# Performance work log

Hardware: AMD Instinct MI355X
Metric: run time of the kernel (lower is better)

## Reference

```python
import jax, jax.numpy as jnp
import numpy as np

HS = 1024
IMS = 4096
NHEAD = 16
EPS = 1e-5


def _layer_norm(x, g, b):
    mu = jnp.mean(x, axis=-1, keepdims=True)
    var = jnp.mean(jnp.square(x - mu), axis=-1, keepdims=True)
    return (x - mu) * jax.lax.rsqrt(var + EPS) * g + b


def setup_inputs() -> dict:
    key = jax.random.key(0)
    ks = jax.random.split(key, 10)
    B, S = 16, 512
    x = jax.random.normal(ks[0], (B, S, HS), dtype=jnp.float32)
    input_mask = jnp.zeros((B, S), dtype=jnp.float32)  # additive mask, 0 = attend
    sc = 0.02
    return {
        "x": x,
        "input_mask": input_mask,
        "qkv_w": jax.random.normal(ks[1], (3 * HS, HS), jnp.float32) * sc,
        "qkv_b": jnp.zeros((3 * HS,), jnp.float32),
        "attn_ow": jax.random.normal(ks[2], (HS, HS), jnp.float32) * sc,
        "attn_ob": jnp.zeros((HS,), jnp.float32),
        "ln1_g": jnp.ones((HS,), jnp.float32),
        "ln1_b": jnp.zeros((HS,), jnp.float32),
        "inter_w": jax.random.normal(ks[3], (IMS, HS), jnp.float32) * sc,
        "inter_b": jnp.zeros((IMS,), jnp.float32),
        "out_w": jax.random.normal(ks[4], (HS, IMS), jnp.float32) * sc,
        "out_b": jnp.zeros((HS,), jnp.float32),
        "ln2_g": jnp.ones((HS,), jnp.float32),
        "ln2_b": jnp.zeros((HS,), jnp.float32),
    }


def reference(x, input_mask, qkv_w, qkv_b, attn_ow, attn_ob, ln1_g, ln1_b,
              inter_w, inter_b, out_w, out_b, ln2_g, ln2_b):
    B, S, H = x.shape
    d = H // NHEAD
    # ---- self-attention block (pre_layer_norm=True, eval mode => no dropout) ----
    resid = x
    y = _layer_norm(x, ln1_g, ln1_b)
    qkv = jnp.einsum('bsh,eh->bse', y, qkv_w) + qkv_b  # [B,S,3H]
    q, k, v = jnp.split(qkv, 3, axis=-1)
    q = q.reshape(B, S, NHEAD, d)
    k = k.reshape(B, S, NHEAD, d)
    v = v.reshape(B, S, NHEAD, d)
    scores = jnp.einsum('bqnd,bknd->bnqk', q, k) / jnp.sqrt(jnp.float32(d))
    scores = scores + input_mask[:, None, None, :]  # additive padding mask
    probs = jax.nn.softmax(scores, axis=-1)
    ctx = jnp.einsum('bnqk,bknd->bqnd', probs, v).reshape(B, S, H)
    attn_out = jnp.einsum('bsh,oh->bso', ctx, attn_ow) + attn_ob
    x = resid + attn_out
    # ---- FFN block ----
    resid = x
    y = _layer_norm(x, ln2_g, ln2_b)
    h = jax.nn.relu(jnp.einsum('bsh,ih->bsi', y, inter_w) + inter_b)
    ffn_out = jnp.einsum('bsi,oi->bso', h, out_w) + out_b
    return resid + ffn_out
```

## Files before the change

### kernel.cpp

```cpp
#include <hip/hip_runtime.h>


using f32x4  = __attribute__((ext_vector_type(4))) float;
using f32x16 = __attribute__((ext_vector_type(16))) float;
using s16x8  = __attribute__((ext_vector_type(8))) short;
using i32x4  = __attribute__((ext_vector_type(4))) int;

__device__ __forceinline__ unsigned short f2bf(float f) {
    unsigned x = __builtin_bit_cast(unsigned, f);
    return (unsigned short)((x + 0x7fffu + ((x >> 16) & 1u)) >> 16);
}

#define GLL16(gptr, lptr)                                                     \
    __builtin_amdgcn_global_load_lds(                                         \
        (const __attribute__((address_space(1))) void*)(gptr),                \
        (__attribute__((address_space(3))) void*)(lptr), 16, 0, 0)

#define VMC(N) asm volatile("s_waitcnt vmcnt(" #N ")" ::: "memory")

__global__ __launch_bounds__(256) void wconv_kernel(
    const float* __restrict__ w0, const float* __restrict__ w1,
    const float* __restrict__ w2, const float* __restrict__ w3,
    unsigned short* __restrict__ o0, unsigned short* __restrict__ o1,
    unsigned short* __restrict__ o2, unsigned short* __restrict__ o3) {
    long idx = (long)blockIdx.x * 256 + threadIdx.x;
    const float* src;
    unsigned short* dst;
    long rel;
    if (idx < 786432L)        { src = w0; dst = o0; rel = idx; }
    else if (idx < 1048576L)  { src = w1; dst = o1; rel = idx - 786432L; }
    else if (idx < 2097152L)  { src = w2; dst = o2; rel = idx - 1048576L; }
    else                      { src = w3; dst = o3; rel = idx - 2097152L; }
    float4 v = *(const float4*)(src + rel * 4);
    ushort4 o;
    o.x = f2bf(v.x); o.y = f2bf(v.y); o.z = f2bf(v.z); o.w = f2bf(v.w);
    *(ushort4*)(dst + rel * 4) = o;
}

__global__ __launch_bounds__(256) void ln_kernel(
    const float* __restrict__ x, const float* __restrict__ gw,
    const float* __restrict__ bw, unsigned short* __restrict__ y) {
    __shared__ float rbuf[8];
    const int row = blockIdx.x;
    const int t = threadIdx.x;
    const float* xr = x + (size_t)row * 1024;
    float4 v = *(const float4*)(xr + t * 4);
    float s  = v.x + v.y + v.z + v.w;
    float ss = v.x * v.x + v.y * v.y + v.z * v.z + v.w * v.w;
#pragma unroll
    for (int sh = 1; sh < 64; sh <<= 1) {
        s  += __shfl_xor(s, sh, 64);
        ss += __shfl_xor(ss, sh, 64);
    }
    int w = t >> 6;
    if ((t & 63) == 0) { rbuf[w * 2] = s; rbuf[w * 2 + 1] = ss; }
    __syncthreads();
    s  = rbuf[0] + rbuf[2] + rbuf[4] + rbuf[6];
    ss = rbuf[1] + rbuf[3] + rbuf[5] + rbuf[7];
    float mu  = s * (1.f / 1024.f);
    float var = ss * (1.f / 1024.f) - mu * mu;
    float rs  = rsqrtf(var + 1e-5f);
    float4 gv = *(const float4*)(gw + t * 4);
    float4 bv = *(const float4*)(bw + t * 4);
    ushort4 o;
    o.x = f2bf((v.x - mu) * rs * gv.x + bv.x);
    o.y = f2bf((v.y - mu) * rs * gv.y + bv.y);
    o.z = f2bf((v.z - mu) * rs * gv.z + bv.z);
    o.w = f2bf((v.w - mu) * rs * gv.w + bv.w);
    *(ushort4*)(y + (size_t)row * 1024 + t * 4) = o;
}

template <bool RELU, bool RESID, bool OUT_BF16>
__global__ __launch_bounds__(256, 2) void gemm_bt(
    const unsigned short* __restrict__ A, const unsigned short* __restrict__ Bw,
    const float* __restrict__ bias, const float* __restrict__ resid,
    void* __restrict__ Cout, int M, int N, int K) {
    __shared__ char smem[2 * 128 * 64 * 2];
    char* As = smem;
    char* Bs = smem + 128 * 64 * 2;

    const int tid = threadIdx.x;
    const int lane = tid & 63;
    const int w = tid >> 6;
    const int wr = w >> 1, wc = w & 1;
    const int g = lane >> 4;
    const int fr = lane & 15;
    const int nwg = gridDim.x * gridDim.y;
    const int L = blockIdx.y * gridDim.x + blockIdx.x;
    const int swz = (L & 7) * (nwg >> 3) + (L >> 3);
    const int m0 = (swz / gridDim.x) * 128;
    const int n0 = (swz % gridDim.x) * 128;

    f32x4 acc[4][4] = {};

    for (int kt = 0; kt < K; kt += 64) {
#pragma unroll
        for (int c = 0; c < 4; ++c) {
            int lin = (c * 256 + tid) * 16;
            int row = lin >> 7;
            int Lb = lin ^ ((row & 7) << 4);
            int colb = Lb & 127;
            const char* ga = (const char*)A + ((size_t)(m0 + row) * K + kt) * 2 + colb;
            const char* gb = (const char*)Bw + ((size_t)(n0 + row) * K + kt) * 2 + colb;
            GLL16(ga, As + lin);
            GLL16(gb, Bs + lin);
        }
        __syncthreads();
#pragma unroll
        for (int ks = 0; ks < 2; ++ks) {
            s16x8 af[4], bf[4];
#pragma unroll
            for (int mi = 0; mi < 4; ++mi) {
                int row = wr * 64 + mi * 16 + fr;
                int off = (row << 7) + ((ks * 64 + g * 16) ^ ((row & 7) << 4));
                af[mi] = *(const s16x8*)(As + off);
            }
#pragma unroll
            for (int ni = 0; ni < 4; ++ni) {
                int row = wc * 64 + ni * 16 + fr;
                int off = (row << 7) + ((ks * 64 + g * 16) ^ ((row & 7) << 4));
                bf[ni] = *(const s16x8*)(Bs + off);
            }
#pragma unroll
            for (int mi = 0; mi < 4; ++mi)
#pragma unroll
                for (int ni = 0; ni < 4; ++ni)
                    acc[mi][ni] = __builtin_amdgcn_mfma_f32_16x16x32_bf16(
                        af[mi], bf[ni], acc[mi][ni], 0, 0, 0);
        }
        __syncthreads();
    }

    float bv[4];
#pragma unroll
    for (int ni = 0; ni < 4; ++ni) bv[ni] = bias[n0 + wc * 64 + ni * 16 + fr];
#pragma unroll
    for (int mi = 0; mi < 4; ++mi) {
#pragma unroll
        for (int r = 0; r < 4; ++r) {
            int row = m0 + wr * 64 + mi * 16 + g * 4 + r;
#pragma unroll
            for (int ni = 0; ni < 4; ++ni) {
                int col = n0 + wc * 64 + ni * 16 + fr;
                float v = acc[mi][ni][r] + bv[ni];
                if (RELU) v = v > 0.f ? v : 0.f;
                if (RESID) v += resid[(size_t)row * N + col];
                if (OUT_BF16)
                    ((unsigned short*)Cout)[(size_t)row * N + col] = f2bf(v);
                else
                    ((float*)Cout)[(size_t)row * N + col] = v;
            }
        }
    }
}

template <bool RELU, bool OUT_BF16>
__global__ __launch_bounds__(512, 2) void gemm256(
    const unsigned short* __restrict__ A, const unsigned short* __restrict__ Bw,
    const float* __restrict__ bias, void* __restrict__ Cout,
    int M, int N, int K) {
    extern __shared__ char lds[];

    const int tid = threadIdx.x;
    const int lane = tid & 63;
    const int w = tid >> 6;
    const int wm = w >> 2, wn = w & 3;
    const int g = lane >> 4, fr = lane & 15;

    const int nwg = gridDim.x * gridDim.y;
    const int L = blockIdx.y * gridDim.x + blockIdx.x;
    const int swz = (L & 7) * (nwg >> 3) + (L >> 3);
    const int m0 = (swz / gridDim.x) * 256;
    const int n0 = (swz % gridDim.x) * 256;

    const int NT = K >> 6;

    auto stageA = [&](int t, int h) {
        char* dst = lds + (t & 1) * 32768 + h * 16384;
#pragma unroll
        for (int c2 = 0; c2 < 2; ++c2) {
            int lin = (c2 * 512 + tid) * 16;
            int row = lin >> 7;
            int colb = (lin & 127) ^ ((row & 7) << 4);
            GLL16((const char*)A + ((size_t)(m0 + h * 128 + row) * K + t * 64) * 2 + colb,
                  dst + lin);
        }
    };
    auto stageB = [&](int t, int h) {
        char* dst = lds + 65536 + (t & 1) * 32768 + h * 16384;
#pragma unroll
        for (int c2 = 0; c2 < 2; ++c2) {
            int lin = (c2 * 512 + tid) * 16;
            int row = lin >> 7;
            int colb = (lin & 127) ^ ((row & 7) << 4);
            GLL16((const char*)Bw + ((size_t)(n0 + h * 128 + row) * K + t * 64) * 2 + colb,
                  dst + lin);
        }
    };

    f32x4 acc[2][4][2][2] = {};
    s16x8 af[4][2];
    s16x8 bf[2][2];

    auto loadA = [&](const char* Ab, int ha) {
#pragma unroll
        for (int mi2 = 0; mi2 < 4; ++mi2) {
            int row = ha * 128 + wm * 64 + mi2 * 16 + fr;
#pragma unroll
            for (int ks = 0; ks < 2; ++ks)
                af[mi2][ks] = *(const s16x8*)(Ab + (row << 7) +
                               ((ks * 64 + g * 16) ^ ((row & 7) << 4)));
        }
    };
    auto loadB = [&](const char* Bb, int hb) {
#pragma unroll
        for (int ni2 = 0; ni2 < 2; ++ni2) {
            int row = hb * 128 + wn * 32 + ni2 * 16 + fr;
#pragma unroll
            for (int ks = 0; ks < 2; ++ks)
                bf[ni2][ks] = *(const s16x8*)(Bb + (row << 7) +
                               ((ks * 64 + g * 16) ^ ((row & 7) << 4)));
        }
    };

#define MFMAQ(HA, HB)                                                         \
    __builtin_amdgcn_s_barrier();                                             \
    asm volatile("s_waitcnt lgkmcnt(0)" ::: "memory");                        \
    __builtin_amdgcn_sched_barrier(0);                                        \
    __builtin_amdgcn_s_setprio(1);                                            \
    _Pragma("unroll")                                                         \
    for (int mi2 = 0; mi2 < 4; ++mi2)                                         \
        _Pragma("unroll")                                                     \
        for (int ni2 = 0; ni2 < 2; ++ni2)                                     \
            _Pragma("unroll")                                                 \
            for (int ks = 0; ks < 2; ++ks)                                    \
                acc[HA][mi2][HB][ni2] =                                       \
                    __builtin_amdgcn_mfma_f32_16x16x32_bf16(                  \
                        af[mi2][ks], bf[ni2][ks], acc[HA][mi2][HB][ni2],      \
                        0, 0, 0);                                             \
    __builtin_amdgcn_s_setprio(0);                                            \
    __builtin_amdgcn_s_barrier();

    stageA(0, 0); stageB(0, 0); stageA(0, 1); stageB(0, 1);
    stageA(1, 0); stageB(1, 0);
    VMC(8);
    __builtin_amdgcn_s_barrier();

    for (int t = 0; t < NT - 2; ++t) {
        char* Ab = lds + (t & 1) * 32768;
        char* Bb = lds + 65536 + (t & 1) * 32768;
        loadA(Ab, 0); loadB(Bb, 0); stageA(t + 1, 1); VMC(6); MFMAQ(0, 0);
        loadB(Bb, 1);               stageB(t + 1, 1);         MFMAQ(0, 1);
        loadA(Ab, 1); loadB(Bb, 0); stageA(t + 2, 0);         MFMAQ(1, 0);
        loadB(Bb, 1);               stageB(t + 2, 0); VMC(8); MFMAQ(1, 1);
    }
    {
        const int t = NT - 2;
        char* Ab = lds + (t & 1) * 32768;
        char* Bb = lds + 65536 + (t & 1) * 32768;
        loadA(Ab, 0); loadB(Bb, 0); stageA(t + 1, 1); VMC(6); MFMAQ(0, 0);
        loadB(Bb, 1);               stageB(t + 1, 1);         MFMAQ(0, 1);
        loadA(Ab, 1); loadB(Bb, 0);                           MFMAQ(1, 0);
        loadB(Bb, 1);                                 VMC(4); MFMAQ(1, 1);
    }
    {
        const int t = NT - 1;
        char* Ab = lds + (t & 1) * 32768;
        char* Bb = lds + 65536 + (t & 1) * 32768;
        loadA(Ab, 0); loadB(Bb, 0);                   VMC(0); MFMAQ(0, 0);
        loadB(Bb, 1);                                         MFMAQ(0, 1);
        loadA(Ab, 1); loadB(Bb, 0);                           MFMAQ(1, 0);
        loadB(Bb, 1);                                         MFMAQ(1, 1);
    }
#undef MFMAQ

#pragma unroll
    for (int ha = 0; ha < 2; ++ha)
#pragma unroll
        for (int mi2 = 0; mi2 < 4; ++mi2)
#pragma unroll
            for (int r = 0; r < 4; ++r) {
                int row = m0 + ha * 128 + wm * 64 + mi2 * 16 + g * 4 + r;
#pragma unroll
                for (int hb = 0; hb < 2; ++hb)
#pragma unroll
                    for (int ni2 = 0; ni2 < 2; ++ni2) {
                        int col = n0 + hb * 128 + wn * 32 + ni2 * 16 + fr;
                        float v = acc[ha][mi2][hb][ni2][r] + bias[col];
                        if (RELU) v = v > 0.f ? v : 0.f;
                        if (OUT_BF16)
                            ((unsigned short*)Cout)[(size_t)row * N + col] = f2bf(v);
                        else
                            ((float*)Cout)[(size_t)row * N + col] = v;
                    }
            }
}

__global__ __launch_bounds__(512, 2) void attn_kernel(
    const unsigned short* __restrict__ qkv, const float* __restrict__ mask,
    unsigned short* __restrict__ ctx) {
    extern __shared__ char smem[];

    const int tid = threadIdx.x;
    const int lane = tid & 63;
    const int w = tid >> 6;
    const int l31 = lane & 31;
    const int hi = lane >> 5;
    const int bh = blockIdx.x >> 1;
    const int b = bh >> 4, h = bh & 15;
    const int qt = (blockIdx.x & 1) * 256 + w * 32;

    const size_t rstr = 3072;
    const unsigned short* qbase = qkv + (size_t)b * 512 * rstr + h * 64;
    const unsigned short* kbase = qbase + 1024;
    const unsigned short* vbase = qbase + 2048;
    const float* mrow = mask + b * 512;

    s16x8 qf[4];
#pragma unroll
    for (int kc = 0; kc < 4; ++kc)
        qf[kc] = *(const s16x8*)(qbase + (size_t)(qt + l31) * rstr + kc * 16 + hi * 8);

    f32x16 O0 = {}, O1 = {};
    float m = -3e38f, l = 0.f;
    const int bpbase = 36 * hi * 4;

    auto stage = [&](int kt, int bufsel) {
        char* Kb = smem + bufsel * 16384;
        char* Vb = smem + 32768 + bufsel * 16384;
#pragma unroll
        for (int c = 0; c < 2; ++c) {
            int lin = (c * 512 + tid) * 16;
            int row = lin >> 7;
            int colb = (lin & 127) ^ ((row & 7) << 4);
            GLL16((const char*)kbase + (size_t)(kt * 128 + row) * rstr * 2 + colb,
                  Kb + lin);
        }
        int s = tid & 127, dg = tid >> 7;
        const unsigned short* vsrc = vbase + (size_t)(kt * 128 + s) * rstr + dg * 16;
        union { i32x4 v; unsigned short u[8]; } v0, v1;
        v0.v = *(const i32x4*)vsrc;
        v1.v = *(const i32x4*)(vsrc + 8);
#pragma unroll
        for (int j = 0; j < 8; ++j) {
            int d = dg * 16 + j;
            *(unsigned short*)(Vb + d * 256 + ((s * 2) ^ ((d & 15) << 4))) = v0.u[j];
        }
#pragma unroll
        for (int j = 0; j < 8; ++j) {
            int d = dg * 16 + 8 + j;
            *(unsigned short*)(Vb + d * 256 + ((s * 2) ^ ((d & 15) << 4))) = v1.u[j];
        }
    };

    const float C   = 0.18033688f;
    const float L2E = 1.44269504f;

    stage(0, 0);
    __syncthreads();

    for (int kt = 0; kt < 4; ++kt) {
        const int cur = kt & 1;
        if (kt < 3) stage(kt + 1, cur ^ 1);
        char* Kb = smem + cur * 16384;
        char* Vb = smem + 32768 + cur * 16384;
        const int swzk = (l31 & 7) << 4;

        f32x16 sc[4];
#pragma unroll
        for (int t = 0; t < 4; ++t) {
            f32x16 a = {};
#pragma unroll
            for (int kc = 0; kc < 4; ++kc) {
                s16x8 kf = *(const s16x8*)(Kb + (32 * t + l31) * 128 +
                                           ((kc * 32 + hi * 16) ^ swzk));
                a = __builtin_amdgcn_mfma_f32_32x32x16_bf16(kf, qf[kc], a, 0, 0, 0);
            }
            sc[t] = a;
        }

        float tm = -3e38f;
#pragma unroll
        for (int t = 0; t < 4; ++t) {
#pragma unroll
            for (int k2 = 0; k2 < 4; ++k2) {
                f32x4 mk = *(const f32x4*)(mrow + kt * 128 + 32 * t + 8 * k2 + 4 * hi);
#pragma unroll
                for (int i = 0; i < 4; ++i) {
                    float v = sc[t][4 * k2 + i] * C + mk[i] * L2E;
                    sc[t][4 * k2 + i] = v;
                    tm = fmaxf(tm, v);
                }
            }
        }
        tm = fmaxf(tm, __shfl_xor(tm, 32, 64));

        if (__any(tm > m + 11.0f)) {
            float mn = fmaxf(m, tm);
            float fac = exp2f(m - mn);
            m = mn;
            l *= fac;
            int fi = __float_as_int(fac);
#pragma unroll
            for (int r = 0; r < 16; ++r) {
                int q2 = (r & 3) + 8 * (r >> 2);
                float fq = __int_as_float(
                    __builtin_amdgcn_ds_bpermute(bpbase + q2 * 4, fi));
                O0[r] *= fq;
                O1[r] *= fq;
            }
        }

        float ts = 0.f;
#pragma unroll
        for (int t = 0; t < 4; ++t)
#pragma unroll
            for (int r = 0; r < 16; ++r) {
                float p = exp2f(sc[t][r] - m);
                sc[t][r] = p;
                ts += p;
            }
        ts += __shfl_xor(ts, 32, 64);
        l += ts;

        unsigned pk01[4][4], pk23[4][4];
#pragma unroll
        for (int t = 0; t < 4; ++t)
#pragma unroll
            for (int k = 0; k < 4; ++k) {
                unsigned r0, r1;
                asm("v_cvt_pk_bf16_f32 %0, %1, %2"
                    : "=v"(r0) : "v"(sc[t][4 * k]), "v"(sc[t][4 * k + 1]));
                asm("v_cvt_pk_bf16_f32 %0, %1, %2"
                    : "=v"(r1) : "v"(sc[t][4 * k + 2]), "v"(sc[t][4 * k + 3]));
                pk01[t][k] = r0;
                pk23[t][k] = r1;
            }

#pragma unroll
        for (int t = 0; t < 4; ++t)
#pragma unroll
            for (int cc = 0; cc < 2; ++cc) {
                unsigned a0 = pk01[t][2 * cc], b0 = pk01[t][2 * cc + 1];
                unsigned c0 = pk23[t][2 * cc], d0 = pk23[t][2 * cc + 1];
                asm("v_permlane32_swap_b32 %0, %1" : "+v"(a0), "+v"(b0));
                asm("v_permlane32_swap_b32 %0, %1" : "+v"(c0), "+v"(d0));
                union { unsigned u[4]; s16x8 v; } pf;
                pf.u[0] = a0;
                pf.u[1] = c0;
                pf.u[2] = b0;
                pf.u[3] = d0;
                const int kc = 2 * t + cc;
                {
                    int row = l31;
                    s16x8 vf = *(const s16x8*)(Vb + row * 256 +
                               ((kc * 32 + hi * 16) ^ ((row & 15) << 4)));
                    O0 = __builtin_amdgcn_mfma_f32_32x32x16_bf16(pf.v, vf, O0, 0, 0, 0);
                }
                {
                    int row = 32 + l31;
                    s16x8 vf = *(const s16x8*)(Vb + row * 256 +
                               ((kc * 32 + hi * 16) ^ ((row & 15) << 4)));
                    O1 = __builtin_amdgcn_mfma_f32_32x32x16_bf16(pf.v, vf, O1, 0, 0, 0);
                }
            }
        __syncthreads();
    }

    const int li = __float_as_int(l);
#pragma unroll
    for (int r = 0; r < 16; ++r) {
        int q2 = (r & 3) + 8 * (r >> 2);
        float lq = __int_as_float(__builtin_amdgcn_ds_bpermute(bpbase + q2 * 4, li));
        float inv = 1.f / lq;
        size_t rowg = (size_t)(b * 512 + qt + q2 + 4 * hi) * 1024 + h * 64;
        ctx[rowg + l31]      = f2bf(O0[r] * inv);
        ctx[rowg + 32 + l31] = f2bf(O1[r] * inv);
    }
}

extern "C" void kernel_launch(void* const* d_in, const int* in_sizes, int n_in,
                              void* d_out, int out_size, void* d_ws, size_t ws_size,
                              hipStream_t stream) {
    const float* x    = (const float*)d_in[0];
    const float* mask = (const float*)d_in[1];
    const float* qkvw = (const float*)d_in[2];
    const float* qkvb = (const float*)d_in[3];
    const float* ow   = (const float*)d_in[4];
    const float* ob   = (const float*)d_in[5];
    const float* ln1g = (const float*)d_in[6];
    const float* ln1b = (const float*)d_in[7];
    const float* iw   = (const float*)d_in[8];
    const float* ib   = (const float*)d_in[9];
    const float* o2w  = (const float*)d_in[10];
    const float* o2b  = (const float*)d_in[11];
    const float* ln2g = (const float*)d_in[12];
    const float* ln2b = (const float*)d_in[13];

    char* ws = (char*)d_ws;
    unsigned short* qkvbuf = (unsigned short*)(ws);
    unsigned short* ybuf   = (unsigned short*)(ws + 50331648);
    unsigned short* cbuf   = (unsigned short*)(ws + 67108864);
    float*          x2     = (float*)(ws + 83886080);
    unsigned short* wq     = (unsigned short*)(ws + 117440512);
    unsigned short* wo     = (unsigned short*)(ws + 123731968);
    unsigned short* wi     = (unsigned short*)(ws + 125829120);
    unsigned short* wo2    = (unsigned short*)(ws + 134217728);
    unsigned short* hbuf   = (unsigned short*)(ws);

    hipFuncSetAttribute(reinterpret_cast<const void*>(attn_kernel),
                        hipFuncAttributeMaxDynamicSharedMemorySize, 65536);
    hipFuncSetAttribute(reinterpret_cast<const void*>(&gemm256<false, true>),
                        hipFuncAttributeMaxDynamicSharedMemorySize, 131072);
    hipFuncSetAttribute(reinterpret_cast<const void*>(&gemm256<true, true>),
                        hipFuncAttributeMaxDynamicSharedMemorySize, 131072);

    wconv_kernel<<<12288, 256, 0, stream>>>(qkvw, ow, iw, o2w, wq, wo, wi, wo2);
    ln_kernel<<<8192, 256, 0, stream>>>(x, ln1g, ln1b, ybuf);
    gemm256<false, true><<<dim3(12, 32), 512, 131072, stream>>>(
        ybuf, wq, qkvb, qkvbuf, 8192, 3072, 1024);
    attn_kernel<<<512, 512, 65536, stream>>>(qkvbuf, mask, cbuf);
    gemm_bt<false, true, false><<<dim3(8, 64), 256, 0, stream>>>(
        cbuf, wo, ob, x, x2, 8192, 1024, 1024);
    ln_kernel<<<8192, 256, 0, stream>>>(x2, ln2g, ln2b, cbuf);
    gemm256<true, true><<<dim3(16, 32), 512, 131072, stream>>>(
        cbuf, wi, ib, hbuf, 8192, 4096, 1024);
    gemm_bt<false, true, false><<<dim3(8, 64), 256, 0, stream>>>(
        hbuf, wo2, o2b, x2, (float*)d_out, 8192, 1024, 4096);
}
```

Baseline: 307.8 us.

## Add triple-buffered 128x256 GEMM for QKV and defer V LDS writes in attention

Adds a new GEMM kernel with 128x256 tiles, a three-stage LDS ring fed by global_load_lds, tile-index swizzling and raised wave priority around the MFMA block, and uses it for the QKV projection instead of the 256x256 kernel. In attention, the V tile's global loads are now issued early into registers and the transposed LDS stores are deferred until after the softmax math, so global latency overlaps with compute. The smaller tile doubles the grid size, and the kernel needs 144KB of LDS, which may limit occupancy to one block per CU despite the launch bounds.

```diff
diff --git a/kernel.cpp b/kernel.cpp
--- a/kernel.cpp
+++ b/kernel.cpp
@@ -296,6 +296,115 @@
             }
 }
 
+template <bool RELU, bool RESID, bool OUT_BF16>
+__global__ __launch_bounds__(512, 2) void gemm_dp(
+    const unsigned short* __restrict__ A, const unsigned short* __restrict__ Bw,
+    const float* __restrict__ bias, const float* __restrict__ resid,
+    void* __restrict__ Cout, int M, int N, int K) {
+    extern __shared__ char lds[];
+
+    const int tid = threadIdx.x;
+    const int lane = tid & 63;
+    const int w = tid >> 6;
+    const int wm = w >> 2, wn = w & 3;
+    const int g = lane >> 4, fr = lane & 15;
+
+    const int nwg = gridDim.x * gridDim.y;
+    const int L = blockIdx.y * gridDim.x + blockIdx.x;
+    const int swz = (L & 7) * (nwg >> 3) + (L >> 3);
+    const int m0 = (swz / gridDim.x) * 128;
+    const int n0 = (swz % gridDim.x) * 256;
+
+    const int NT = K >> 6;
+
+    auto stage = [&](int t) {
+        char* dst = lds + (t % 3) * 49152;
+#pragma unroll
+        for (int c = 0; c < 2; ++c) {
+            int lin = (c * 512 + tid) * 16;
+            int row = lin >> 7;
+            int colb = (lin & 127) ^ ((row & 7) << 4);
+            GLL16((const char*)A + ((size_t)(m0 + row) * K + t * 64) * 2 + colb,
+                  dst + lin);
+        }
+#pragma unroll
+        for (int c = 0; c < 4; ++c) {
+            int lin = (c * 512 + tid) * 16;
+            int row = lin >> 7;
+            int colb = (lin & 127) ^ ((row & 7) << 4);
+            GLL16((const char*)Bw + ((size_t)(n0 + row) * K + t * 64) * 2 + colb,
+                  dst + 16384 + lin);
+        }
+    };
+
+    f32x4 acc[4][4] = {};
+
+    stage(0);
+    stage(1);
+    VMC(6);
+    __builtin_amdgcn_s_barrier();
+
+    for (int t = 0; t < NT; ++t) {
+        char* Ab = lds + (t % 3) * 49152;
+        char* Bb = Ab + 16384;
+        s16x8 af[4][2], bf[4][2];
+#pragma unroll
+        for (int mi = 0; mi < 4; ++mi) {
+            int row = wm * 64 + mi * 16 + fr;
+#pragma unroll
+            for (int ks = 0; ks < 2; ++ks)
+                af[mi][ks] = *(const s16x8*)(Ab + (row << 7) +
+                              ((ks * 64 + g * 16) ^ ((row & 7) << 4)));
+        }
+#pragma unroll
+        for (int ni = 0; ni < 4; ++ni) {
+            int row = wn * 64 + ni * 16 + fr;
+#pragma unroll
+            for (int ks = 0; ks < 2; ++ks)
+                bf[ni][ks] = *(const s16x8*)(Bb + (row << 7) +
+                              ((ks * 64 + g * 16) ^ ((row & 7) << 4)));
+        }
+        if (t + 2 < NT) { stage(t + 2); VMC(6); }
+        else if (t + 1 < NT) { VMC(0); }
+        __builtin_amdgcn_s_barrier();
+        asm volatile("s_waitcnt lgkmcnt(0)" ::: "memory");
+        __builtin_amdgcn_sched_barrier(0);
+        __builtin_amdgcn_s_setprio(1);
+#pragma unroll
+        for (int mi = 0; mi < 4; ++mi)
+#pragma unroll
+            for (int ni = 0; ni < 4; ++ni)
+#pragma unroll
+                for (int ks = 0; ks < 2; ++ks)
+                    acc[mi][ni] = __builtin_amdgcn_mfma_f32_16x16x32_bf16(
+                        af[mi][ks], bf[ni][ks], acc[mi][ni], 0, 0, 0);
+        __builtin_amdgcn_s_setprio(0);
+        __builtin_amdgcn_s_barrier();
+    }
+
+    float bv[4];
+#pragma unroll
+    for (int ni = 0; ni < 4; ++ni) bv[ni] = bias[n0 + wn * 64 + ni * 16 + fr];
+#pragma unroll
+    for (int mi = 0; mi < 4; ++mi) {
+#pragma unroll
+        for (int r = 0; r < 4; ++r) {
+            int row = m0 + wm * 64 + mi * 16 + g * 4 + r;
+#pragma unroll
+            for (int ni = 0; ni < 4; ++ni) {
+                int col = n0 + wn * 64 + ni * 16 + fr;
+                float v = acc[mi][ni][r] + bv[ni];
+                if (RELU) v = v > 0.f ? v : 0.f;
+                if (RESID) v += resid[(size_t)row * N + col];
+                if (OUT_BF16)
+                    ((unsigned short*)Cout)[(size_t)row * N + col] = f2bf(v);
+                else
+                    ((float*)Cout)[(size_t)row * N + col] = v;
+            }
+        }
+    }
+}
+
 __global__ __launch_bounds__(512, 2) void attn_kernel(
     const unsigned short* __restrict__ qkv, const float* __restrict__ mask,
     unsigned short* __restrict__ ctx) {
@@ -325,9 +434,16 @@
     float m = -3e38f, l = 0.f;
     const int bpbase = 36 * hi * 4;
 
-    auto stage = [&](int kt, int bufsel) {
+    const int vs = tid & 127, vdg = tid >> 7;
+    i32x4 vr0, vr1;
+
+    auto issueV = [&](int kt) {
+        const unsigned short* vsrc = vbase + (size_t)(kt * 128 + vs) * rstr + vdg * 16;
+        vr0 = *(const i32x4*)vsrc;
+        vr1 = *(const i32x4*)(vsrc + 8);
+    };
+    auto issueK = [&](int kt, int bufsel) {
         char* Kb = smem + bufsel * 16384;
-        char* Vb = smem + 32768 + bufsel * 16384;
 #pragma unroll
         for (int c = 0; c < 2; ++c) {
             int lin = (c * 512 + tid) * 16;
@@ -336,32 +452,33 @@
             GLL16((const char*)kbase + (size_t)(kt * 128 + row) * rstr * 2 + colb,
                   Kb + lin);
         }
-        int s = tid & 127, dg = tid >> 7;
-        const unsigned short* vsrc = vbase + (size_t)(kt * 128 + s) * rstr + dg * 16;
-        union { i32x4 v; unsigned short u[8]; } v0, v1;
-        v0.v = *(const i32x4*)vsrc;
-        v1.v = *(const i32x4*)(vsrc + 8);
+    };
+    auto writeV = [&](int bufsel) {
+        char* Vb = smem + 32768 + bufsel * 16384;
+        union { i32x4 v; unsigned short u[8]; } u0, u1;
+        u0.v = vr0; u1.v = vr1;
 #pragma unroll
         for (int j = 0; j < 8; ++j) {
-            int d = dg * 16 + j;
-            *(unsigned short*)(Vb + d * 256 + ((s * 2) ^ ((d & 15) << 4))) = v0.u[j];
+            int d = vdg * 16 + j;
+            *(unsigned short*)(Vb + d * 256 + ((vs * 2) ^ ((d & 15) << 4))) = u0.u[j];
         }
 #pragma unroll
         for (int j = 0; j < 8; ++j) {
-            int d = dg * 16 + 8 + j;
-            *(unsigned short*)(Vb + d * 256 + ((s * 2) ^ ((d & 15) << 4))) = v1.u[j];
+            int d = vdg * 16 + 8 + j;
+            *(unsigned short*)(Vb + d * 256 + ((vs * 2) ^ ((d & 15) << 4))) = u1.u[j];
         }
     };
 
     const float C   = 0.18033688f;
     const float L2E = 1.44269504f;
 
-    stage(0, 0);
+    issueV(0); issueK(0, 0);
+    writeV(0);
     __syncthreads();
 
     for (int kt = 0; kt < 4; ++kt) {
         const int cur = kt & 1;
-        if (kt < 3) stage(kt + 1, cur ^ 1);
+        if (kt < 3) { issueV(kt + 1); issueK(kt + 1, cur ^ 1); }
         char* Kb = smem + cur * 16384;
         char* Vb = smem + 32768 + cur * 16384;
         const int swzk = (l31 & 7) << 4;
@@ -422,6 +539,8 @@
             }
         ts += __shfl_xor(ts, 32, 64);
         l += ts;
+
+        if (kt < 3) writeV(cur ^ 1);
 
         unsigned pk01[4][4], pk23[4][4];
 #pragma unroll
@@ -510,15 +629,15 @@
 
     hipFuncSetAttribute(reinterpret_cast<const void*>(attn_kernel),
                         hipFuncAttributeMaxDynamicSharedMemorySize, 65536);
-    hipFuncSetAttribute(reinterpret_cast<const void*>(&gemm256<false, true>),
-                        hipFuncAttributeMaxDynamicSharedMemorySize, 131072);
+    hipFuncSetAttribute(reinterpret_cast<const void*>(&gemm_dp<false, false, true>),
+                        hipFuncAttributeMaxDynamicSharedMemorySize, 147456);
     hipFuncSetAttribute(reinterpret_cast<const void*>(&gemm256<true, true>),
                         hipFuncAttributeMaxDynamicSharedMemorySize, 131072);
 
     wconv_kernel<<<12288, 256, 0, stream>>>(qkvw, ow, iw, o2w, wq, wo, wi, wo2);
     ln_kernel<<<8192, 256, 0, stream>>>(x, ln1g, ln1b, ybuf);
-    gemm256<false, true><<<dim3(12, 32), 512, 131072, stream>>>(
-        ybuf, wq, qkvb, qkvbuf, 8192, 3072, 1024);
+    gemm_dp<false, false, true><<<dim3(12, 64), 512, 147456, stream>>>(
+        ybuf, wq, qkvb, nullptr, qkvbuf, 8192, 3072, 1024);
     attn_kernel<<<512, 512, 65536, stream>>>(qkvbuf, mask, cbuf);
     gemm_bt<false, true, false><<<dim3(8, 64), 256, 0, stream>>>(
         cbuf, wo, ob, x, x2, 8192, 1024, 1024);
```

New measurement: 305.5 us. Within noise of the previous version (-0.7%).
